# Kernel optimization log

Hardware: AMD Instinct MI355X
Metric: run time of the kernel (lower is better)

Reference implementation:

```python
import jax, jax.numpy as jnp
import numpy as np

N = 50000      # nodes
E = 800000     # edges (avg degree 16)
IN = 128       # in_features
H = 4          # num_heads
OUT = 32       # out_features per head
NEG_SLOPE = 0.2


def setup_inputs() -> dict:
    key = jax.random.key(0)
    k1, k2, k3, k4 = jax.random.split(key, 4)
    h = jax.random.normal(k1, (N, IN), dtype=jnp.float32)
    edge_index = jax.random.randint(k2, (2, E), 0, N, dtype=jnp.int32)
    # xavier-ish init scales
    W = jax.random.normal(k3, (H, IN, OUT), dtype=jnp.float32) * np.float32(np.sqrt(2.0 / (IN + OUT)))
    a = jax.random.normal(k4, (H, 2 * OUT), dtype=jnp.float32) * np.float32(np.sqrt(2.0 / (2 * OUT)))
    return {"h": h, "edge_index": edge_index, "W": W, "a": a}


def reference(h, edge_index, W, a):
    src, dst = edge_index[0], edge_index[1]
    # project per head: [N, H, OUT]
    h_proj = jnp.einsum('ni,hio->nho', h, W)
    # score = leaky_relu(a . [Wh_src || Wh_dst]) ; split a to avoid materializing the concat
    a_src, a_dst = a[:, :OUT], a[:, OUT:]
    s_src = jnp.einsum('nho,ho->nh', h_proj, a_src)   # [N, H]
    s_dst = jnp.einsum('nho,ho->nh', h_proj, a_dst)   # [N, H]
    score = jax.nn.leaky_relu(s_src[src] + s_dst[dst], negative_slope=NEG_SLOPE)  # [E, H]
    # sparse softmax over incoming edges of each dst node
    smax = jax.ops.segment_max(score, dst, num_segments=N)          # [N, H]
    smax = jnp.where(jnp.isfinite(smax), smax, jnp.float32(-1e9))   # nodes with no in-edges
    score_exp = jnp.exp(score - smax[dst])                          # [E, H]
    denom = jax.ops.segment_sum(score_exp, dst, num_segments=N)     # [N, H]
    denom = jnp.maximum(denom, jnp.float32(1e-16))
    alpha = score_exp / denom[dst]                                  # [E, H]
    # weighted aggregation (dropout is identity in eval mode)
    h_src = h_proj[src]                                             # [E, H, OUT]
    h_out = jax.ops.segment_sum(alpha[:, :, None] * h_src, dst, num_segments=N)  # [N, H, OUT]
    h_out = h_out.reshape(N, H * OUT)  # concat=True
    return jax.nn.elu(h_out)
```

## Files before the change

### kernel.cpp

```cpp
#include <hip/hip_runtime.h>

#define NEG_SLOPE 0.2f
#define BCAP 8192

typedef __attribute__((ext_vector_type(8))) short short8;
typedef __attribute__((ext_vector_type(4))) float floatx4;

__device__ __forceinline__ unsigned f2bf(float x) {
  unsigned u = __float_as_uint(x);
  unsigned r = ((u >> 16) & 1u) + 0x7fffu;
  return (u + r) >> 16;
}
__device__ __forceinline__ float bf2f(unsigned hi16) {
  return __uint_as_float(hi16 << 16);
}

__global__ __launch_bounds__(256) void k_prep(const float* __restrict__ W,
                                              uint4* __restrict__ gWf,
                                              int* __restrict__ bcur, int NB2) {
  if (blockIdx.x == 0 && threadIdx.x < NB2) bcur[threadIdx.x] = 0;
  const int u = blockIdx.x * 256 + threadIdx.x;
  if (u >= 2048) return;
  int ln = u & 63;
  int kc = (u >> 6) & 3;
  int ct = u >> 8;
  int n = ct * 16 + (ln & 15);
  int kb = kc * 32 + (ln >> 4) * 8;
  int head = n >> 5;
  const float* src = W + head * 4096 + (size_t)kb * 32 + (n & 31);
  unsigned hi[4], lo[4];
#pragma unroll
  for (int jj = 0; jj < 4; ++jj) {
    float w0 = src[(2 * jj) * 32];
    float w1 = src[(2 * jj + 1) * 32];
    unsigned h0 = f2bf(w0), h1 = f2bf(w1);
    unsigned l0 = f2bf(w0 - bf2f(h0)), l1 = f2bf(w1 - bf2f(h1));
    hi[jj] = h0 | (h1 << 16);
    lo[jj] = l0 | (l1 << 16);
  }
  gWf[u] = make_uint4(hi[0], hi[1], hi[2], hi[3]);
  gWf[2048 + u] = make_uint4(lo[0], lo[1], lo[2], lo[3]);
}

__global__ __launch_bounds__(256) void k_gemm(const float* __restrict__ h,
                                              const uint4* __restrict__ gWf,
                                              const float* __restrict__ a,
                                              const int* __restrict__ ei,
                                              int* __restrict__ bcur,
                                              uint2* __restrict__ gpairs,
                                              unsigned short* __restrict__ hp16,
                                              float* __restrict__ ssrc,
                                              float* __restrict__ sdst,
                                              int N, int E, int NB1, int NB2) {
  __shared__ unsigned lds_u[16384];
  const int tid = threadIdx.x;

  if (blockIdx.x < NB1) {
    uint2* stage = (uint2*)lds_u;
    int* cnt = (int*)&lds_u[8192];
    int* start = (int*)&lds_u[8448];
    int* cur = (int*)&lds_u[8704];
    int* gbase = (int*)&lds_u[8960];
    int* scn = (int*)&lds_u[9216];
    const int e0 = blockIdx.x * 4096;
    for (int i = tid; i < NB2; i += 256) cnt[i] = 0;
    __syncthreads();
    int sarr[16], darr[16];
#pragma unroll
    for (int j = 0; j < 16; ++j) {
      int e = e0 + j * 256 + tid;
      if (e < E) {
        sarr[j] = ei[e];
        darr[j] = ei[E + e];
        atomicAdd(&cnt[darr[j] >> 8], 1);
      } else {
        darr[j] = -1;
      }
    }
    __syncthreads();
    int s = (tid < NB2) ? cnt[tid] : 0;
    scn[tid] = s;
    __syncthreads();
    for (int off = 1; off < 256; off <<= 1) {
      int t = (tid >= off) ? scn[tid - off] : 0;
      __syncthreads();
      scn[tid] += t;
      __syncthreads();
    }
    if (tid < NB2) {
      start[tid] = scn[tid] - s;
      cur[tid] = scn[tid] - s;
      gbase[tid] = s ? atomicAdd(&bcur[tid], s) : 0;
    }
    __syncthreads();
#pragma unroll
    for (int j = 0; j < 16; ++j) {
      if (darr[j] >= 0) {
        int b = darr[j] >> 8;
        int pos = atomicAdd(&cur[b], 1);
        stage[pos] = make_uint2((unsigned)sarr[j], (unsigned)darr[j]);
      }
    }
    __syncthreads();
    const int total = start[NB2 - 1] + cnt[NB2 - 1];
    for (int u = tid; u < total; u += 256) {
      uint2 pr = stage[u];
      int b = (int)(pr.y >> 8);
      gpairs[(size_t)b * BCAP + gbase[b] + (u - start[b])] = pr;
    }
    __syncthreads();
  }

  const int lane = tid & 63;
  const int wv = tid >> 6;
  const int quad = lane >> 4;
  const int l16 = lane & 15;

  for (int u = tid; u < 4096; u += 256)
    *(uint4*)&lds_u[u * 4] = gWf[u];

  const int row0 = blockIdx.x * 64;
  const int r = row0 + wv * 16 + l16;
  short8 Ah[4], Al[4];
#pragma unroll
  for (int kc = 0; kc < 4; ++kc) {
    float v[8];
    if (r < N) {
      float4 fa = *(const float4*)&h[(size_t)r * 128 + kc * 32 + quad * 8];
      float4 fb = *(const float4*)&h[(size_t)r * 128 + kc * 32 + quad * 8 + 4];
      v[0] = fa.x; v[1] = fa.y; v[2] = fa.z; v[3] = fa.w;
      v[4] = fb.x; v[5] = fb.y; v[6] = fb.z; v[7] = fb.w;
    } else {
#pragma unroll
      for (int j = 0; j < 8; ++j) v[j] = 0.f;
    }
#pragma unroll
    for (int j = 0; j < 8; ++j) {
      unsigned hi = f2bf(v[j]);
      Ah[kc][j] = (short)hi;
      Al[kc][j] = (short)f2bf(v[j] - bf2f(hi));
    }
  }
  __syncthreads();

  floatx4 C[8];
#pragma unroll
  for (int ct = 0; ct < 8; ++ct) {
    floatx4 c = {0.f, 0.f, 0.f, 0.f};
#pragma unroll
    for (int kc = 0; kc < 4; ++kc) {
      int bidx = ((ct * 4 + kc) * 64 + lane) * 4;
      short8 Bh, Bl;
      *(uint4*)&Bh = *(const uint4*)&lds_u[bidx];
      *(uint4*)&Bl = *(const uint4*)&lds_u[8192 + bidx];
      c = __builtin_amdgcn_mfma_f32_16x16x32_bf16(Ah[kc], Bh, c, 0, 0, 0);
      c = __builtin_amdgcn_mfma_f32_16x16x32_bf16(Al[kc], Bh, c, 0, 0, 0);
      c = __builtin_amdgcn_mfma_f32_16x16x32_bf16(Ah[kc], Bl, c, 0, 0, 0);
    }
    C[ct] = c;
  }
  __syncthreads();

  float* epi = (float*)lds_u;
#pragma unroll
  for (int ct = 0; ct < 8; ++ct) {
#pragma unroll
    for (int reg = 0; reg < 4; ++reg) {
      int rr = wv * 16 + quad * 4 + reg;
      epi[rr * 132 + ct * 16 + l16] = C[ct][reg];
    }
  }
  __syncthreads();

  const int row_l = tid >> 2;
  const int hh = tid & 3;
  const int rg = row0 + row_l;
  if (rg < N) {
    const float* rowp = &epi[row_l * 132 + hh * 32];
    float ss = 0.f, sd = 0.f;
    unsigned pka[16];
#pragma unroll
    for (int e = 0; e < 8; ++e) {
      float4 c4 = *(const float4*)&rowp[e * 4];
      float4 as = *(const float4*)&a[hh * 64 + e * 4];
      float4 ad = *(const float4*)&a[hh * 64 + 32 + e * 4];
      ss += c4.x * as.x + c4.y * as.y + c4.z * as.z + c4.w * as.w;
      sd += c4.x * ad.x + c4.y * ad.y + c4.z * ad.z + c4.w * ad.w;
      pka[e * 2] = f2bf(c4.x) | (f2bf(c4.y) << 16);
      pka[e * 2 + 1] = f2bf(c4.z) | (f2bf(c4.w) << 16);
    }
    unsigned short* dst = &hp16[(size_t)rg * 128 + hh * 32];
    *(uint4*)(dst) = make_uint4(pka[0], pka[1], pka[2], pka[3]);
    *(uint4*)(dst + 8) = make_uint4(pka[4], pka[5], pka[6], pka[7]);
    *(uint4*)(dst + 16) = make_uint4(pka[8], pka[9], pka[10], pka[11]);
    *(uint4*)(dst + 24) = make_uint4(pka[12], pka[13], pka[14], pka[15]);
    ssrc[(size_t)rg * 4 + hh] = ss;
    sdst[(size_t)rg * 4 + hh] = sd;
  }
}

__global__ __launch_bounds__(256) void k_build(const int* __restrict__ bcur,
                                               const uint2* __restrict__ gpairs,
                                               const float* __restrict__ ssrc,
                                               const float* __restrict__ sdst,
                                               int* __restrict__ csr_src,
                                               float4* __restrict__ escore,
                                               int2* __restrict__ offs2, int N) {
  __shared__ int cnt2[256], start2[256], cur2[256];
  __shared__ int lds[256];
  __shared__ int srcsort[BCAP];
  const int tid = threadIdx.x;
  const int b = blockIdx.x;
  const size_t base = (size_t)b * BCAP;
  const int size = bcur[b];
  const int d0 = b << 8;
  const int ndst = min(256, N - d0);
  cnt2[tid] = 0;
  __syncthreads();
  for (int u = tid; u < size; u += 256)
    atomicAdd(&cnt2[(int)gpairs[base + u].y - d0], 1);
  __syncthreads();
  {
    int s = cnt2[tid];
    lds[tid] = s;
    __syncthreads();
    for (int off = 1; off < 256; off <<= 1) {
      int t = (tid >= off) ? lds[tid - off] : 0;
      __syncthreads();
      lds[tid] += t;
      __syncthreads();
    }
    start2[tid] = lds[tid] - s;
    cur2[tid] = lds[tid] - s;
  }
  __syncthreads();
  for (int u = tid; u < size; u += 256) {
    uint2 pr = gpairs[base + u];
    int d = (int)pr.y;
    int pos = atomicAdd(&cur2[d - d0], 1);
    int s = (int)pr.x;
    srcsort[pos] = s;
    float4 sv = *(const float4*)&ssrc[(size_t)s * 4];
    float4 dv = *(const float4*)&sdst[(size_t)d * 4];
    float4 w;
    float x;
    x = sv.x + dv.x; x = x >= 0.f ? x : NEG_SLOPE * x; w.x = __expf(x);
    x = sv.y + dv.y; x = x >= 0.f ? x : NEG_SLOPE * x; w.y = __expf(x);
    x = sv.z + dv.z; x = x >= 0.f ? x : NEG_SLOPE * x; w.z = __expf(x);
    x = sv.w + dv.w; x = x >= 0.f ? x : NEG_SLOPE * x; w.w = __expf(x);
    escore[base + pos] = w;
  }
  __syncthreads();
  for (int u = tid; u < size; u += 256) csr_src[base + u] = srcsort[u];
  if (tid < ndst) {
    int beg = (int)base + start2[tid];
    offs2[d0 + tid] = make_int2(beg, beg + cnt2[tid]);
  }
}

__global__ __launch_bounds__(256) void k_agg(const int2* __restrict__ offs2,
                                             const int* __restrict__ csr_src,
                                             const float* __restrict__ escore,
                                             const uint4* __restrict__ hp4,
                                             float* __restrict__ out, int N) {
  const int t = blockIdx.x * 256 + threadIdx.x;
  const int d = t >> 4;
  if (d >= N) return;
  const int l = threadIdx.x & 15;
  const int hh = l >> 2;
  const int2 be = offs2[d];
  const int beg = be.x, end = be.y;

  float den[4] = {0.f, 0.f, 0.f, 0.f};
  float acc[8];
#pragma unroll
  for (int j = 0; j < 8; ++j) acc[j] = 0.f;

  int p = beg;
  for (; p + 3 < end; p += 4) {
    int s[4];
    float w[4];
    uint4 v[4];
#pragma unroll
    for (int q = 0; q < 4; ++q) s[q] = csr_src[p + q];
#pragma unroll
    for (int q = 0; q < 4; ++q) {
      w[q] = escore[(size_t)(p + q) * 4 + hh];
      v[q] = hp4[(size_t)s[q] * 16 + l];
    }
#pragma unroll
    for (int q = 0; q < 4; ++q) {
      den[q] += w[q];
      acc[0] = fmaf(w[q], bf2f(v[q].x & 0xffffu), acc[0]);
      acc[1] = fmaf(w[q], bf2f(v[q].x >> 16), acc[1]);
      acc[2] = fmaf(w[q], bf2f(v[q].y & 0xffffu), acc[2]);
      acc[3] = fmaf(w[q], bf2f(v[q].y >> 16), acc[3]);
      acc[4] = fmaf(w[q], bf2f(v[q].z & 0xffffu), acc[4]);
      acc[5] = fmaf(w[q], bf2f(v[q].z >> 16), acc[5]);
      acc[6] = fmaf(w[q], bf2f(v[q].w & 0xffffu), acc[6]);
      acc[7] = fmaf(w[q], bf2f(v[q].w >> 16), acc[7]);
    }
  }
  for (; p < end; ++p) {
    int s0 = csr_src[p];
    float w0 = escore[(size_t)p * 4 + hh];
    uint4 v0 = hp4[(size_t)s0 * 16 + l];
    den[0] += w0;
    acc[0] = fmaf(w0, bf2f(v0.x & 0xffffu), acc[0]);
    acc[1] = fmaf(w0, bf2f(v0.x >> 16), acc[1]);
    acc[2] = fmaf(w0, bf2f(v0.y & 0xffffu), acc[2]);
    acc[3] = fmaf(w0, bf2f(v0.y >> 16), acc[3]);
    acc[4] = fmaf(w0, bf2f(v0.z & 0xffffu), acc[4]);
    acc[5] = fmaf(w0, bf2f(v0.z >> 16), acc[5]);
    acc[6] = fmaf(w0, bf2f(v0.w & 0xffffu), acc[6]);
    acc[7] = fmaf(w0, bf2f(v0.w >> 16), acc[7]);
  }
  float rden = 1.f / fmaxf((den[0] + den[1]) + (den[2] + den[3]), 1e-16f);
  float o[8];
#pragma unroll
  for (int j = 0; j < 8; ++j) {
    float x = acc[j] * rden;
    o[j] = x > 0.f ? x : expm1f(x);
  }
  float* dst = &out[(size_t)d * 128 + l * 8];
  *(float4*)dst = make_float4(o[0], o[1], o[2], o[3]);
  *(float4*)(dst + 4) = make_float4(o[4], o[5], o[6], o[7]);
}

extern "C" void kernel_launch(void* const* d_in, const int* in_sizes, int n_in,
                              void* d_out, int out_size, void* d_ws, size_t ws_size,
                              hipStream_t stream) {
  const float* h = (const float*)d_in[0];
  const int* ei = (const int*)d_in[1];
  const float* W = (const float*)d_in[2];
  const float* a = (const float*)d_in[3];
  float* out = (float*)d_out;
  const int N = in_sizes[0] / 128;
  const int E = in_sizes[1] / 2;
  const int NB2 = (N + 255) >> 8;
  const int NB1 = (E + 4095) / 4096;
  const int NBG = max((N + 63) / 64, NB1);

  char* ws = (char*)d_ws;
  uint4* gWf = (uint4*)ws;
  unsigned short* hp16 = (unsigned short*)(gWf + 4096);
  uint2* gpairs = (uint2*)(hp16 + (size_t)N * 128);
  float4* escore = (float4*)(gpairs + (size_t)NB2 * BCAP);
  int2* offs2 = (int2*)(escore + (size_t)NB2 * BCAP);
  float* ssrc = (float*)(offs2 + N);
  float* sdst = ssrc + (size_t)N * 4;
  int* bcur = (int*)(sdst + (size_t)N * 4);
  int* csr_src = bcur + NB2;

  k_prep<<<8, 256, 0, stream>>>(W, gWf, bcur, NB2);
  k_gemm<<<NBG, 256, 0, stream>>>(h, gWf, a, ei, bcur, gpairs, hp16, ssrc, sdst,
                                  N, E, NB1, NB2);
  k_build<<<NB2, 256, 0, stream>>>(bcur, gpairs, ssrc, sdst, csr_src, escore, offs2, N);
  k_agg<<<(N * 16 + 255) / 256, 256, 0, stream>>>(offs2, csr_src, (const float*)escore,
                                                  (const uint4*)hp16, out, N);
}
```

Before: 159.8 us.

## Fuse bucket sort and aggregation into one LDS-resident kernel

Merges the CSR build and aggregation kernels into a single 1024-thread kernel per 256-destination bucket. The sorted source list stays in LDS, and edge weights are recomputed during aggregation from ssrc and an LDS copy of sdst, so the escore, csr_src and offs2 global arrays are no longer written or read back. This removes one launch and a large amount of global traffic. In exchange only about 196 blocks of 1024 threads run, which may leave parallelism thin for the gather-heavy aggregation. Buckets larger than BCAP are now silently truncated.

```diff
diff --git a/kernel.cpp b/kernel.cpp
--- a/kernel.cpp
+++ b/kernel.cpp
@@ -199,132 +199,128 @@
   }
 }
 
-__global__ __launch_bounds__(256) void k_build(const int* __restrict__ bcur,
-                                               const uint2* __restrict__ gpairs,
-                                               const float* __restrict__ ssrc,
-                                               const float* __restrict__ sdst,
-                                               int* __restrict__ csr_src,
-                                               float4* __restrict__ escore,
-                                               int2* __restrict__ offs2, int N) {
-  __shared__ int cnt2[256], start2[256], cur2[256];
-  __shared__ int lds[256];
+__global__ __launch_bounds__(1024) void k_sortagg(const int* __restrict__ bcur,
+                                                  const uint2* __restrict__ gpairs,
+                                                  const float* __restrict__ ssrc,
+                                                  const float* __restrict__ sdst,
+                                                  const uint4* __restrict__ hp4,
+                                                  float* __restrict__ out, int N) {
+  __shared__ int cnt2[256], start2[256], cur2[256], lds[256];
   __shared__ int srcsort[BCAP];
+  __shared__ float sdl[1024];
   const int tid = threadIdx.x;
   const int b = blockIdx.x;
   const size_t base = (size_t)b * BCAP;
-  const int size = bcur[b];
+  const int size = min(bcur[b], BCAP);
   const int d0 = b << 8;
   const int ndst = min(256, N - d0);
-  cnt2[tid] = 0;
-  __syncthreads();
-  for (int u = tid; u < size; u += 256)
-    atomicAdd(&cnt2[(int)gpairs[base + u].y - d0], 1);
-  __syncthreads();
-  {
-    int s = cnt2[tid];
-    lds[tid] = s;
-    __syncthreads();
-    for (int off = 1; off < 256; off <<= 1) {
-      int t = (tid >= off) ? lds[tid - off] : 0;
-      __syncthreads();
-      lds[tid] += t;
-      __syncthreads();
-    }
-    start2[tid] = lds[tid] - s;
-    cur2[tid] = lds[tid] - s;
-  }
-  __syncthreads();
-  for (int u = tid; u < size; u += 256) {
-    uint2 pr = gpairs[base + u];
-    int d = (int)pr.y;
-    int pos = atomicAdd(&cur2[d - d0], 1);
-    int s = (int)pr.x;
-    srcsort[pos] = s;
-    float4 sv = *(const float4*)&ssrc[(size_t)s * 4];
-    float4 dv = *(const float4*)&sdst[(size_t)d * 4];
-    float4 w;
-    float x;
-    x = sv.x + dv.x; x = x >= 0.f ? x : NEG_SLOPE * x; w.x = __expf(x);
-    x = sv.y + dv.y; x = x >= 0.f ? x : NEG_SLOPE * x; w.y = __expf(x);
-    x = sv.z + dv.z; x = x >= 0.f ? x : NEG_SLOPE * x; w.z = __expf(x);
-    x = sv.w + dv.w; x = x >= 0.f ? x : NEG_SLOPE * x; w.w = __expf(x);
-    escore[base + pos] = w;
-  }
-  __syncthreads();
-  for (int u = tid; u < size; u += 256) csr_src[base + u] = srcsort[u];
-  if (tid < ndst) {
-    int beg = (int)base + start2[tid];
-    offs2[d0 + tid] = make_int2(beg, beg + cnt2[tid]);
-  }
-}
-
-__global__ __launch_bounds__(256) void k_agg(const int2* __restrict__ offs2,
-                                             const int* __restrict__ csr_src,
-                                             const float* __restrict__ escore,
-                                             const uint4* __restrict__ hp4,
-                                             float* __restrict__ out, int N) {
-  const int t = blockIdx.x * 256 + threadIdx.x;
-  const int d = t >> 4;
-  if (d >= N) return;
-  const int l = threadIdx.x & 15;
+
+  if (tid < 256) cnt2[tid] = 0;
+  for (int i = tid; i < ndst * 4; i += 1024) sdl[i] = sdst[(size_t)d0 * 4 + i];
+  __syncthreads();
+
+  uint2 pr[8];
+#pragma unroll
+  for (int j = 0; j < 8; ++j) {
+    const int u = tid + j * 1024;
+    if (u < size) pr[j] = gpairs[base + u];
+    else pr[j].y = 0xffffffffu;
+  }
+#pragma unroll
+  for (int j = 0; j < 8; ++j)
+    if (pr[j].y != 0xffffffffu) atomicAdd(&cnt2[(int)pr[j].y - d0], 1);
+  __syncthreads();
+
+  if (tid < 256) lds[tid] = cnt2[tid];
+  __syncthreads();
+  for (int off = 1; off < 256; off <<= 1) {
+    const int t = (tid < 256 && tid >= off) ? lds[tid - off] : 0;
+    __syncthreads();
+    if (tid < 256) lds[tid] += t;
+    __syncthreads();
+  }
+  if (tid < 256) {
+    start2[tid] = lds[tid] - cnt2[tid];
+    cur2[tid] = lds[tid] - cnt2[tid];
+  }
+  __syncthreads();
+
+#pragma unroll
+  for (int j = 0; j < 8; ++j) {
+    if (pr[j].y != 0xffffffffu) {
+      const int pos = atomicAdd(&cur2[(int)pr[j].y - d0], 1);
+      srcsort[pos] = (int)pr[j].x;
+    }
+  }
+  __syncthreads();
+
+  const int l = tid & 15;
   const int hh = l >> 2;
-  const int2 be = offs2[d];
-  const int beg = be.x, end = be.y;
-
-  float den[4] = {0.f, 0.f, 0.f, 0.f};
-  float acc[8];
-#pragma unroll
-  for (int j = 0; j < 8; ++j) acc[j] = 0.f;
-
-  int p = beg;
-  for (; p + 3 < end; p += 4) {
-    int s[4];
-    float w[4];
-    uint4 v[4];
-#pragma unroll
-    for (int q = 0; q < 4; ++q) s[q] = csr_src[p + q];
-#pragma unroll
-    for (int q = 0; q < 4; ++q) {
-      w[q] = escore[(size_t)(p + q) * 4 + hh];
-      v[q] = hp4[(size_t)s[q] * 16 + l];
-    }
-#pragma unroll
-    for (int q = 0; q < 4; ++q) {
-      den[q] += w[q];
-      acc[0] = fmaf(w[q], bf2f(v[q].x & 0xffffu), acc[0]);
-      acc[1] = fmaf(w[q], bf2f(v[q].x >> 16), acc[1]);
-      acc[2] = fmaf(w[q], bf2f(v[q].y & 0xffffu), acc[2]);
-      acc[3] = fmaf(w[q], bf2f(v[q].y >> 16), acc[3]);
-      acc[4] = fmaf(w[q], bf2f(v[q].z & 0xffffu), acc[4]);
-      acc[5] = fmaf(w[q], bf2f(v[q].z >> 16), acc[5]);
-      acc[6] = fmaf(w[q], bf2f(v[q].w & 0xffffu), acc[6]);
-      acc[7] = fmaf(w[q], bf2f(v[q].w >> 16), acc[7]);
-    }
-  }
-  for (; p < end; ++p) {
-    int s0 = csr_src[p];
-    float w0 = escore[(size_t)p * 4 + hh];
-    uint4 v0 = hp4[(size_t)s0 * 16 + l];
-    den[0] += w0;
-    acc[0] = fmaf(w0, bf2f(v0.x & 0xffffu), acc[0]);
-    acc[1] = fmaf(w0, bf2f(v0.x >> 16), acc[1]);
-    acc[2] = fmaf(w0, bf2f(v0.y & 0xffffu), acc[2]);
-    acc[3] = fmaf(w0, bf2f(v0.y >> 16), acc[3]);
-    acc[4] = fmaf(w0, bf2f(v0.z & 0xffffu), acc[4]);
-    acc[5] = fmaf(w0, bf2f(v0.z >> 16), acc[5]);
-    acc[6] = fmaf(w0, bf2f(v0.w & 0xffffu), acc[6]);
-    acc[7] = fmaf(w0, bf2f(v0.w >> 16), acc[7]);
-  }
-  float rden = 1.f / fmaxf((den[0] + den[1]) + (den[2] + den[3]), 1e-16f);
-  float o[8];
-#pragma unroll
-  for (int j = 0; j < 8; ++j) {
-    float x = acc[j] * rden;
-    o[j] = x > 0.f ? x : expm1f(x);
-  }
-  float* dst = &out[(size_t)d * 128 + l * 8];
-  *(float4*)dst = make_float4(o[0], o[1], o[2], o[3]);
-  *(float4*)(dst + 4) = make_float4(o[4], o[5], o[6], o[7]);
+  for (int dl = tid >> 4; dl < ndst; dl += 64) {
+    const int d = d0 + dl;
+    const int beg = start2[dl];
+    const int end = beg + cnt2[dl];
+    const float sdv = sdl[dl * 4 + hh];
+
+    float den[4] = {0.f, 0.f, 0.f, 0.f};
+    float acc[8];
+#pragma unroll
+    for (int j = 0; j < 8; ++j) acc[j] = 0.f;
+
+    int p = beg;
+    for (; p + 3 < end; p += 4) {
+      int s[4];
+      float w[4];
+      uint4 v[4];
+#pragma unroll
+      for (int q = 0; q < 4; ++q) s[q] = srcsort[p + q];
+#pragma unroll
+      for (int q = 0; q < 4; ++q) {
+        float x = ssrc[(size_t)s[q] * 4 + hh] + sdv;
+        x = x >= 0.f ? x : NEG_SLOPE * x;
+        w[q] = __expf(x);
+        v[q] = hp4[(size_t)s[q] * 16 + l];
+      }
+#pragma unroll
+      for (int q = 0; q < 4; ++q) {
+        den[q] += w[q];
+        acc[0] = fmaf(w[q], bf2f(v[q].x & 0xffffu), acc[0]);
+        acc[1] = fmaf(w[q], bf2f(v[q].x >> 16), acc[1]);
+        acc[2] = fmaf(w[q], bf2f(v[q].y & 0xffffu), acc[2]);
+        acc[3] = fmaf(w[q], bf2f(v[q].y >> 16), acc[3]);
+        acc[4] = fmaf(w[q], bf2f(v[q].z & 0xffffu), acc[4]);
+        acc[5] = fmaf(w[q], bf2f(v[q].z >> 16), acc[5]);
+        acc[6] = fmaf(w[q], bf2f(v[q].w & 0xffffu), acc[6]);
+        acc[7] = fmaf(w[q], bf2f(v[q].w >> 16), acc[7]);
+      }
+    }
+    for (; p < end; ++p) {
+      const int s0 = srcsort[p];
+      float x = ssrc[(size_t)s0 * 4 + hh] + sdv;
+      x = x >= 0.f ? x : NEG_SLOPE * x;
+      const float w0 = __expf(x);
+      const uint4 v0 = hp4[(size_t)s0 * 16 + l];
+      den[0] += w0;
+      acc[0] = fmaf(w0, bf2f(v0.x & 0xffffu), acc[0]);
+      acc[1] = fmaf(w0, bf2f(v0.x >> 16), acc[1]);
+      acc[2] = fmaf(w0, bf2f(v0.y & 0xffffu), acc[2]);
+      acc[3] = fmaf(w0, bf2f(v0.y >> 16), acc[3]);
+      acc[4] = fmaf(w0, bf2f(v0.z & 0xffffu), acc[4]);
+      acc[5] = fmaf(w0, bf2f(v0.z >> 16), acc[5]);
+      acc[6] = fmaf(w0, bf2f(v0.w & 0xffffu), acc[6]);
+      acc[7] = fmaf(w0, bf2f(v0.w >> 16), acc[7]);
+    }
+    const float rden = 1.f / fmaxf((den[0] + den[1]) + (den[2] + den[3]), 1e-16f);
+    float o[8];
+#pragma unroll
+    for (int j = 0; j < 8; ++j) {
+      const float x = acc[j] * rden;
+      o[j] = x > 0.f ? x : expm1f(x);
+    }
+    float* dst = &out[(size_t)d * 128 + l * 8];
+    *(float4*)dst = make_float4(o[0], o[1], o[2], o[3]);
+    *(float4*)(dst + 4) = make_float4(o[4], o[5], o[6], o[7]);
+  }
 }
 
 extern "C" void kernel_launch(void* const* d_in, const int* in_sizes, int n_in,
@@ -345,17 +341,13 @@
   uint4* gWf = (uint4*)ws;
   unsigned short* hp16 = (unsigned short*)(gWf + 4096);
   uint2* gpairs = (uint2*)(hp16 + (size_t)N * 128);
-  float4* escore = (float4*)(gpairs + (size_t)NB2 * BCAP);
-  int2* offs2 = (int2*)(escore + (size_t)NB2 * BCAP);
-  float* ssrc = (float*)(offs2 + N);
+  float* ssrc = (float*)(gpairs + (size_t)NB2 * BCAP);
   float* sdst = ssrc + (size_t)N * 4;
   int* bcur = (int*)(sdst + (size_t)N * 4);
-  int* csr_src = bcur + NB2;
 
   k_prep<<<8, 256, 0, stream>>>(W, gWf, bcur, NB2);
   k_gemm<<<NBG, 256, 0, stream>>>(h, gWf, a, ei, bcur, gpairs, hp16, ssrc, sdst,
                                   N, E, NB1, NB2);
-  k_build<<<NB2, 256, 0, stream>>>(bcur, gpairs, ssrc, sdst, csr_src, escore, offs2, N);
-  k_agg<<<(N * 16 + 255) / 256, 256, 0, stream>>>(offs2, csr_src, (const float*)escore,
-                                                  (const uint4*)hp16, out, N);
-}
+  k_sortagg<<<NB2, 1024, 0, stream>>>(bcur, gpairs, ssrc, sdst,
+                                      (const uint4*)hp16, out, N);
+}
```

Measured after the change: 143.8 us. 1.11x faster.
